# Performance work log

Hardware: AMD Instinct MI355X
Metric: run time of the kernel (lower is better)

The kernel has to match this reference:

```python
import jax, jax.numpy as jnp
import numpy as np

IN_DIM = 256
OUT_DIM = 64
NUM_HEADS = 4
N = 6144


def setup_inputs() -> dict:
    key = jax.random.key(0)
    ks = jax.random.split(key, 9)
    h = jax.random.normal(ks[0], (N, IN_DIM), dtype=jnp.float32)
    # dense multiplicative adjacency weights, one [N,N] matrix per head
    adj = jax.random.uniform(ks[1], (NUM_HEADS, N, N), dtype=jnp.float32)
    s = 1.0 / np.sqrt(IN_DIM)
    WQ = jax.random.normal(ks[2], (NUM_HEADS, IN_DIM, OUT_DIM), dtype=jnp.float32) * s
    WK = jax.random.normal(ks[3], (NUM_HEADS, IN_DIM, OUT_DIM), dtype=jnp.float32) * s
    WV = jax.random.normal(ks[4], (NUM_HEADS, IN_DIM, OUT_DIM), dtype=jnp.float32) * s
    bQ = jax.random.normal(ks[5], (NUM_HEADS, OUT_DIM), dtype=jnp.float32) * 0.01
    bK = jax.random.normal(ks[6], (NUM_HEADS, OUT_DIM), dtype=jnp.float32) * 0.01
    bV = jax.random.normal(ks[7], (NUM_HEADS, OUT_DIM), dtype=jnp.float32) * 0.01
    return {"adj": adj, "h": h, "WQ": WQ, "bQ": bQ, "WK": WK, "bK": bK, "WV": WV, "bV": bV}


def reference(adj, h, WQ, bQ, WK, bK, WV, bV):
    # Per-head projections, batched over heads: [H, N, out_dim]
    Qh = jnp.einsum('nd,hdo->hno', h, WQ) + bQ[:, None, :]
    Kh = jnp.einsum('nd,hdo->hno', h, WK) + bK[:, None, :]
    Vh = jnp.einsum('nd,hdo->hno', h, WV) + bV[:, None, :]
    scale = 1.0 / jnp.sqrt(jnp.asarray(h.shape[1], dtype=h.dtype))
    # multiplicative adjacency mask (NOT additive) applied before softmax
    A_tilde = scale * jnp.einsum('hno,hmo->hnm', Qh, Kh) * adj  # [H, N, N]
    attention = jax.nn.softmax(A_tilde, axis=-1)
    X = jnp.einsum('hnm,hmo->hno', attention, Vh)  # [H, N, out_dim]
    return X
```

## Files before the change

kernel.cpp:

```cpp
#include <hip/hip_runtime.h>
#include <hip/hip_bf16.h>

#define NN 6144
#define HEADS 4
#define DIN 256
#define DOUT 64

typedef __bf16 bf16_t;
typedef bf16_t bf16x8 __attribute__((ext_vector_type(8)));
typedef float f32x16 __attribute__((ext_vector_type(16)));
typedef float f32x4 __attribute__((ext_vector_type(4)));
typedef unsigned u32x4 __attribute__((ext_vector_type(4)));

#if __has_builtin(__builtin_amdgcn_exp2f)
#define EXP2(x) __builtin_amdgcn_exp2f(x)
#else
#define EXP2(x) exp2f(x)
#endif

static __device__ __forceinline__ f32x16 zero16() {
  f32x16 z;
#pragma unroll
  for (int i = 0; i < 16; ++i) z[i] = 0.0f;
  return z;
}

static __device__ __forceinline__ bf16x8 ldg8(const bf16_t* p) {
  return *reinterpret_cast<const bf16x8*>(p);
}

static __device__ __forceinline__ unsigned pk2(float a, float b) {
  union { bf16_t h[2]; unsigned u; } z;
  z.h[0] = (bf16_t)a;
  z.h[1] = (bf16_t)b;
  return z.u;
}

static __device__ __forceinline__ void pswap(unsigned& x, unsigned& y) {
  asm("v_permlane32_swap_b32 %0, %1" : "+v"(x), "+v"(y));
}

static __device__ __forceinline__ void gload_lds16(const float* g, float* lds) {
  __builtin_amdgcn_global_load_lds(
      (const __attribute__((address_space(1))) unsigned*)(uintptr_t)g,
      (__attribute__((address_space(3))) unsigned*)(unsigned)(uintptr_t)lds,
      16, 0, 0);
}

__global__ __launch_bounds__(256) void prep_kernel(
    const float* __restrict__ h, const float* __restrict__ WQ,
    const float* __restrict__ WK, const float* __restrict__ WV,
    bf16_t* __restrict__ hb, bf16_t* __restrict__ Wt) {
  int stride = gridDim.x * blockDim.x;
  int idx = blockIdx.x * blockDim.x + threadIdx.x;
  for (int i = idx; i < NN * DIN; i += stride)
    hb[i] = (bf16_t)h[i];
  const float c2 = 0.0625f * 1.4426950408889634f;
  for (int i = idx; i < 3 * HEADS * DOUT * DIN; i += stride) {
    int d = i & (DIN - 1);
    int o = (i >> 8) & (DOUT - 1);
    int hh = (i >> 14) & (HEADS - 1);
    int m = i >> 16;
    const float* W = (m == 0) ? WQ : (m == 1) ? WK : WV;
    float v = W[(hh * DIN + d) * DOUT + o];
    if (m == 0) v *= c2;
    Wt[i] = (bf16_t)v;
  }
}

__global__ __launch_bounds__(256) void proj_kernel(
    const bf16_t* __restrict__ hb, const bf16_t* __restrict__ Wt,
    const float* __restrict__ bQ, const float* __restrict__ bK,
    const float* __restrict__ bV,
    bf16_t* __restrict__ Qb, bf16_t* __restrict__ Kf, bf16_t* __restrict__ Vf) {
  const float c2 = 0.0625f * 1.4426950408889634f;
  int tid = threadIdx.x;
  int w = tid >> 6, l = tid & 63;
  int l31 = l & 31, lh = l >> 5;
  int hh = blockIdx.y;
  int n0 = blockIdx.x * 64;

#pragma unroll
  for (int s = 0; s < 3; ++s) {
    int t = w * 3 + s;
    if (t < 8) {
      int m = t >> 2;
      int rh = (t >> 1) & 1;
      int oh = t & 1;
      const bf16_t* arow = hb + (n0 + rh * 32 + l31) * DIN + 8 * lh;
      const bf16_t* brow = Wt + ((m * HEADS + hh) * DOUT + oh * 32 + l31) * DIN + 8 * lh;
      f32x16 acc = zero16();
#pragma unroll
      for (int kc = 0; kc < 16; ++kc)
        acc = __builtin_amdgcn_mfma_f32_32x32x16_bf16(ldg8(arow + kc * 16),
                                                      ldg8(brow + kc * 16), acc, 0, 0, 0);
      const float* bias = (m == 0) ? bQ : bK;
      float bv = bias[hh * DOUT + oh * 32 + l31];
      if (m == 0) {
        bv *= c2;
        bf16_t* outp = Qb + (size_t)(hh * NN + n0 + rh * 32) * DOUT + oh * 32 + l31;
#pragma unroll
        for (int r = 0; r < 16; ++r) {
          int q = (r & 3) + 8 * (r >> 2) + 4 * lh;
          outp[q * DOUT] = (bf16_t)(acc[r] + bv);
        }
      } else {
        int o = oh * 32 + l31;
        bf16_t* outp = Kf + (size_t)hh * 393216 + (n0 >> 6) * 4096 + rh * 2048 +
                       (o >> 4) * 512 + ((o >> 3) & 1) * 256 + (o & 7);
#pragma unroll
        for (int r = 0; r < 16; ++r) {
          int rr = (r & 3) + 8 * (r >> 2) + 4 * lh;
          outp[rr * 8] = (bf16_t)(acc[r] + bv);
        }
      }
    } else {
      int tt = t - 8;
      int oh = tt >> 1, nh = tt & 1;
      const bf16_t* arow = Wt + ((2 * HEADS + hh) * DOUT + oh * 32 + l31) * DIN + 8 * lh;
      const bf16_t* brow = hb + (n0 + nh * 32 + l31) * DIN + 8 * lh;
      f32x16 acc = zero16();
#pragma unroll
      for (int kc = 0; kc < 16; ++kc)
        acc = __builtin_amdgcn_mfma_f32_32x32x16_bf16(ldg8(arow + kc * 16),
                                                      ldg8(brow + kc * 16), acc, 0, 0, 0);
      int keyloc = nh * 32 + l31;
      bf16_t* outp = Vf + (size_t)hh * 393216 + (n0 >> 6) * 4096 + oh * 2048 +
                     (keyloc >> 4) * 512 + ((keyloc >> 3) & 1) * 256 + (keyloc & 7);
#pragma unroll
      for (int r = 0; r < 16; ++r) {
        int rr = (r & 3) + 8 * (r >> 2) + 4 * lh;
        float bvv = bV[hh * DOUT + oh * 32 + rr];
        outp[rr * 8] = (bf16_t)(acc[r] + bvv);
      }
    }
  }
}

__global__ __launch_bounds__(256, 2) void attn_kernel(
    const float* __restrict__ adj, const bf16_t* __restrict__ Qb,
    const bf16_t* __restrict__ Kf, const bf16_t* __restrict__ Vf,
    float* __restrict__ out) {
  __shared__ __align__(16) float smem[2][32][256];

  int tid = threadIdx.x;
  int w = tid >> 6, l = tid & 63;
  int l31 = l & 31, lh = l >> 5;
  int hh = blockIdx.y;
  int q0 = blockIdx.x * 32;

  const bf16_t* Qrow = Qb + (size_t)(hh * NN + q0 + l31) * DOUT + 8 * lh;
  bf16x8 qf[4];
#pragma unroll
  for (int kc = 0; kc < 4; ++kc) qf[kc] = ldg8(Qrow + kc * 16);

  const bf16_t* Kh = Kf + (size_t)hh * 393216;
  const bf16_t* Vh = Vf + (size_t)hh * 393216;
  const float* adjq = adj + (size_t)hh * NN * NN + (size_t)q0 * NN;

  f32x16 o0 = zero16(), o1 = zero16();
  float sacc = 0.0f;

#pragma unroll
  for (int i = 0; i < 8; ++i) {
    int row = 8 * w + i;
    gload_lds16(adjq + (size_t)row * NN + ((l ^ i) << 2), &smem[0][row][0]);
  }

  for (int it = 0; it < 24; ++it) {
    int cur = it & 1;
    int chunk = it * 4 + w;

    const bf16_t* kbase = Kh + (size_t)chunk * 4096 + l * 8;
    const bf16_t* vbase = Vh + (size_t)chunk * 4096 + l * 8;
    bf16x8 kf[8], vf[8];
#pragma unroll
    for (int x = 0; x < 4; ++x) {
      kf[x] = ldg8(kbase + x * 512);
      kf[4 + x] = ldg8(kbase + 2048 + x * 512);
    }
#pragma unroll
    for (int x = 0; x < 4; ++x) {
      vf[x] = ldg8(vbase + x * 512);
      vf[4 + x] = ldg8(vbase + 2048 + x * 512);
    }
    __builtin_amdgcn_sched_barrier(0);

    asm volatile("s_waitcnt vmcnt(16)" ::: "memory");
    __builtin_amdgcn_sched_barrier(0);
    __builtin_amdgcn_s_barrier();
    __builtin_amdgcn_sched_barrier(0);

    int nt = (it + 1 < 24) ? it + 1 : 23;
#pragma unroll
    for (int i = 0; i < 8; ++i) {
      int row = 8 * w + i;
      gload_lds16(adjq + (size_t)row * NN + nt * 256 + ((l ^ i) << 2),
                  &smem[cur ^ 1][row][0]);
    }
    __builtin_amdgcn_sched_barrier(0);

    f32x4 av[8];
#pragma unroll
    for (int t2 = 0; t2 < 2; ++t2)
#pragma unroll
      for (int g = 0; g < 4; ++g) {
        int c = 16 * w + 8 * t2 + 2 * g + lh;
        av[t2 * 4 + g] =
            *reinterpret_cast<const f32x4*>(&smem[cur][l31][(c ^ (l31 & 7)) << 2]);
      }

    f32x16 s0 = zero16(), s1 = zero16();
#pragma unroll
    for (int kc = 0; kc < 4; ++kc) {
      s0 = __builtin_amdgcn_mfma_f32_32x32x16_bf16(kf[kc], qf[kc], s0, 0, 0, 0);
      s1 = __builtin_amdgcn_mfma_f32_32x32x16_bf16(kf[4 + kc], qf[kc], s1, 0, 0, 0);
    }

#pragma unroll
    for (int t2 = 0; t2 < 2; ++t2) {
      f32x16 st = t2 ? s1 : s0;
      float p[16];
#pragma unroll
      for (int r = 0; r < 16; ++r) {
        float pv = EXP2(st[r] * av[4 * t2 + (r >> 2)][r & 3]);
        p[r] = pv;
        sacc += pv;
      }
#pragma unroll
      for (int c = 0; c < 2; ++c) {
        unsigned wA0 = pk2(p[8 * c + 0], p[8 * c + 1]);
        unsigned wB0 = pk2(p[8 * c + 2], p[8 * c + 3]);
        unsigned wA1 = pk2(p[8 * c + 4], p[8 * c + 5]);
        unsigned wB1 = pk2(p[8 * c + 6], p[8 * c + 7]);
        pswap(wA0, wA1);
        pswap(wB0, wB1);
        u32x4 pw;
        pw[0] = wA0; pw[1] = wB0; pw[2] = wA1; pw[3] = wB1;
        bf16x8 pb = __builtin_bit_cast(bf16x8, pw);
        int kc = 2 * t2 + c;
        o0 = __builtin_amdgcn_mfma_f32_32x32x16_bf16(vf[kc], pb, o0, 0, 0, 0);
        o1 = __builtin_amdgcn_mfma_f32_32x32x16_bf16(vf[4 + kc], pb, o1, 0, 0, 0);
      }
    }
  }

  asm volatile("s_waitcnt vmcnt(0)" ::: "memory");
  __syncthreads();

  float stot = sacc + __shfl_xor(sacc, 32);
  float* opart = &smem[0][0][0];
  float* ssum = &smem[0][0][0] + 8192;
  if (l < 32) ssum[w * 32 + l31] = stot;
#pragma unroll
  for (int r = 0; r < 16; ++r) {
    int d = (r & 3) + 8 * (r >> 2) + 4 * lh;
    opart[w * 2048 + d * 32 + l31] = o0[r];
    opart[w * 2048 + (32 + d) * 32 + l31] = o1[r];
  }
  __syncthreads();

#pragma unroll
  for (int k = 0; k < 8; ++k) {
    int idx = k * 256 + tid;
    int q = idx & 31, d = idx >> 5;
    float s = ssum[q] + ssum[32 + q] + ssum[64 + q] + ssum[96 + q];
    float ov = opart[d * 32 + q] + opart[2048 + d * 32 + q] +
               opart[4096 + d * 32 + q] + opart[6144 + d * 32 + q];
    out[(size_t)(hh * NN + q0 + q) * DOUT + d] = ov / s;
  }
}

extern "C" void kernel_launch(void* const* d_in, const int* in_sizes, int n_in,
                              void* d_out, int out_size, void* d_ws, size_t ws_size,
                              hipStream_t stream) {
  const float* adj = (const float*)d_in[0];
  const float* h   = (const float*)d_in[1];
  const float* WQ  = (const float*)d_in[2];
  const float* bQ  = (const float*)d_in[3];
  const float* WK  = (const float*)d_in[4];
  const float* bK  = (const float*)d_in[5];
  const float* WV  = (const float*)d_in[6];
  const float* bV  = (const float*)d_in[7];
  float* out = (float*)d_out;

  if (ws_size < 12976128) return;

  char* ws = (char*)d_ws;
  bf16_t* hb = (bf16_t*)ws;
  bf16_t* Wt = (bf16_t*)(ws + 3145728);
  bf16_t* Qb = (bf16_t*)(ws + 3538944);
  bf16_t* Kf = (bf16_t*)(ws + 6684672);
  bf16_t* Vf = (bf16_t*)(ws + 9830400);

  prep_kernel<<<1024, 256, 0, stream>>>(h, WQ, WK, WV, hb, Wt);
  proj_kernel<<<dim3(96, 4), 256, 0, stream>>>(hb, Wt, bQ, bK, bV, Qb, Kf, Vf);
  attn_kernel<<<dim3(192, 4), 256, 0, stream>>>(adj, Qb, Kf, Vf, out);
}
```

Measured before the change: 188.0 us.

## Split attention key range across single-wave blocks with atomic accumulation and normalize pass

```diff
diff --git a/kernel.cpp b/kernel.cpp
--- a/kernel.cpp
+++ b/kernel.cpp
@@ -50,11 +50,13 @@
 __global__ __launch_bounds__(256) void prep_kernel(
     const float* __restrict__ h, const float* __restrict__ WQ,
     const float* __restrict__ WK, const float* __restrict__ WV,
-    bf16_t* __restrict__ hb, bf16_t* __restrict__ Wt) {
+    bf16_t* __restrict__ hb, bf16_t* __restrict__ Wt,
+    float* __restrict__ out, float* __restrict__ denom) {
   int stride = gridDim.x * blockDim.x;
   int idx = blockIdx.x * blockDim.x + threadIdx.x;
-  for (int i = idx; i < NN * DIN; i += stride)
-    hb[i] = (bf16_t)h[i];
+  for (int i = idx; i < HEADS * NN * DOUT; i += stride) out[i] = 0.0f;
+  for (int i = idx; i < HEADS * NN; i += stride) denom[i] = 0.0f;
+  for (int i = idx; i < NN * DIN; i += stride) hb[i] = (bf16_t)h[i];
   const float c2 = 0.0625f * 1.4426950408889634f;
   for (int i = idx; i < 3 * HEADS * DOUT * DIN; i += stride) {
     int d = i & (DIN - 1);
@@ -124,9 +126,9 @@
       for (int kc = 0; kc < 16; ++kc)
         acc = __builtin_amdgcn_mfma_f32_32x32x16_bf16(ldg8(arow + kc * 16),
                                                       ldg8(brow + kc * 16), acc, 0, 0, 0);
-      int keyloc = nh * 32 + l31;
+      int k6 = nh * 32 + l31;
       bf16_t* outp = Vf + (size_t)hh * 393216 + (n0 >> 6) * 4096 + oh * 2048 +
-                     (keyloc >> 4) * 512 + ((keyloc >> 3) & 1) * 256 + (keyloc & 7);
+                     (k6 >> 4) * 512 + ((k6 >> 3) & 1) * 256 + (k6 & 7);
 #pragma unroll
       for (int r = 0; r < 16; ++r) {
         int rr = (r & 3) + 8 * (r >> 2) + 4 * lh;
@@ -137,17 +139,23 @@
   }
 }
 
-__global__ __launch_bounds__(256, 2) void attn_kernel(
+__global__ __launch_bounds__(64, 2) void attn_kernel(
     const float* __restrict__ adj, const bf16_t* __restrict__ Qb,
     const bf16_t* __restrict__ Kf, const bf16_t* __restrict__ Vf,
-    float* __restrict__ out) {
-  __shared__ __align__(16) float smem[2][32][256];
-
-  int tid = threadIdx.x;
-  int w = tid >> 6, l = tid & 63;
+    float* __restrict__ out, float* __restrict__ denom) {
+  __shared__ __align__(16) float tile[2][32][64];
+
+  int l = threadIdx.x;
   int l31 = l & 31, lh = l >> 5;
-  int hh = blockIdx.y;
-  int q0 = blockIdx.x * 32;
+
+  int bid = blockIdx.x;
+  int sb = (bid & 7) * 384 + (bid >> 3);
+  int bx = sb % 192;
+  int rem = sb / 192;
+  int ky = rem & 3;
+  int hh = rem >> 2;
+  int q0 = bx * 32;
+  int ck0 = ky * 24;
 
   const bf16_t* Qrow = Qb + (size_t)(hh * NN + q0 + l31) * DOUT + 8 * lh;
   bf16x8 qf[4];
@@ -156,20 +164,24 @@
 
   const bf16_t* Kh = Kf + (size_t)hh * 393216;
   const bf16_t* Vh = Vf + (size_t)hh * 393216;
-  const float* adjq = adj + (size_t)hh * NN * NN + (size_t)q0 * NN;
+  const float* adjbase = adj + (size_t)(hh * NN + q0) * NN + ky * 1536;
+
+#define STAGE(BUF, CK)                                                      \
+  _Pragma("unroll") for (int i = 0; i < 8; ++i) {                           \
+    int row = 4 * i + (l >> 4);                                             \
+    int sc = (l & 15) ^ (row & 15);                                         \
+    gload_lds16(adjbase + (size_t)row * NN + (CK) * 64 + sc * 4,            \
+                &tile[BUF][4 * i][0]);                                      \
+  }
 
   f32x16 o0 = zero16(), o1 = zero16();
   float sacc = 0.0f;
 
-#pragma unroll
-  for (int i = 0; i < 8; ++i) {
-    int row = 8 * w + i;
-    gload_lds16(adjq + (size_t)row * NN + ((l ^ i) << 2), &smem[0][row][0]);
-  }
+  STAGE(0, 0)
 
   for (int it = 0; it < 24; ++it) {
-    int cur = it & 1;
-    int chunk = it * 4 + w;
+    int buf = it & 1;
+    int chunk = ck0 + it;
 
     const bf16_t* kbase = Kh + (size_t)chunk * 4096 + l * 8;
     const bf16_t* vbase = Vh + (size_t)chunk * 4096 + l * 8;
@@ -186,28 +198,21 @@
     }
     __builtin_amdgcn_sched_barrier(0);
 
-    asm volatile("s_waitcnt vmcnt(16)" ::: "memory");
+    int nt = (it + 1 < 24) ? it + 1 : 23;
+    STAGE(buf ^ 1, nt)
     __builtin_amdgcn_sched_barrier(0);
-    __builtin_amdgcn_s_barrier();
+
+    asm volatile("s_waitcnt vmcnt(24)" ::: "memory");
     __builtin_amdgcn_sched_barrier(0);
 
-    int nt = (it + 1 < 24) ? it + 1 : 23;
-#pragma unroll
-    for (int i = 0; i < 8; ++i) {
-      int row = 8 * w + i;
-      gload_lds16(adjq + (size_t)row * NN + nt * 256 + ((l ^ i) << 2),
-                  &smem[cur ^ 1][row][0]);
-    }
-    __builtin_amdgcn_sched_barrier(0);
-
     f32x4 av[8];
 #pragma unroll
     for (int t2 = 0; t2 < 2; ++t2)
 #pragma unroll
       for (int g = 0; g < 4; ++g) {
-        int c = 16 * w + 8 * t2 + 2 * g + lh;
+        int c = 8 * t2 + 2 * g + lh;
         av[t2 * 4 + g] =
-            *reinterpret_cast<const f32x4*>(&smem[cur][l31][(c ^ (l31 & 7)) << 2]);
+            *reinterpret_cast<const f32x4*>(&tile[buf][l31][(c ^ (l31 & 15)) << 2]);
       }
 
     f32x16 s0 = zero16(), s1 = zero16();
@@ -239,36 +244,33 @@
         pw[0] = wA0; pw[1] = wB0; pw[2] = wA1; pw[3] = wB1;
         bf16x8 pb = __builtin_bit_cast(bf16x8, pw);
         int kc = 2 * t2 + c;
-        o0 = __builtin_amdgcn_mfma_f32_32x32x16_bf16(vf[kc], pb, o0, 0, 0, 0);
-        o1 = __builtin_amdgcn_mfma_f32_32x32x16_bf16(vf[4 + kc], pb, o1, 0, 0, 0);
-      }
-    }
-  }
-
-  asm volatile("s_waitcnt vmcnt(0)" ::: "memory");
-  __syncthreads();
+        o0 = __builtin_amdgcn_mfma_f32_32x32x16_bf16(pb, vf[kc], o0, 0, 0, 0);
+        o1 = __builtin_amdgcn_mfma_f32_32x32x16_bf16(pb, vf[4 + kc], o1, 0, 0, 0);
+      }
+    }
+  }
 
   float stot = sacc + __shfl_xor(sacc, 32);
-  float* opart = &smem[0][0][0];
-  float* ssum = &smem[0][0][0] + 8192;
-  if (l < 32) ssum[w * 32 + l31] = stot;
+  if (l < 32) atomicAdd(&denom[hh * NN + q0 + l31], stot);
 #pragma unroll
   for (int r = 0; r < 16; ++r) {
-    int d = (r & 3) + 8 * (r >> 2) + 4 * lh;
-    opart[w * 2048 + d * 32 + l31] = o0[r];
-    opart[w * 2048 + (32 + d) * 32 + l31] = o1[r];
-  }
-  __syncthreads();
-
-#pragma unroll
-  for (int k = 0; k < 8; ++k) {
-    int idx = k * 256 + tid;
-    int q = idx & 31, d = idx >> 5;
-    float s = ssum[q] + ssum[32 + q] + ssum[64 + q] + ssum[96 + q];
-    float ov = opart[d * 32 + q] + opart[2048 + d * 32 + q] +
-               opart[4096 + d * 32 + q] + opart[6144 + d * 32 + q];
-    out[(size_t)(hh * NN + q0 + q) * DOUT + d] = ov / s;
-  }
+    int q = (r & 3) + 8 * (r >> 2) + 4 * lh;
+    size_t base = (size_t)(hh * NN + q0 + q) * DOUT;
+    atomicAdd(&out[base + l31], o0[r]);
+    atomicAdd(&out[base + 32 + l31], o1[r]);
+  }
+#undef STAGE
+}
+
+__global__ __launch_bounds__(256) void norm_kernel(
+    float* __restrict__ out, const float* __restrict__ denom) {
+  int i = blockIdx.x * 256 + threadIdx.x;
+  float dn = denom[i >> 4];
+  f32x4 v = reinterpret_cast<f32x4*>(out)[i];
+  float inv = 1.0f / dn;
+#pragma unroll
+  for (int j = 0; j < 4; ++j) v[j] *= inv;
+  reinterpret_cast<f32x4*>(out)[i] = v;
 }
 
 extern "C" void kernel_launch(void* const* d_in, const int* in_sizes, int n_in,
@@ -284,16 +286,18 @@
   const float* bV  = (const float*)d_in[7];
   float* out = (float*)d_out;
 
-  if (ws_size < 12976128) return;
+  if (ws_size < 13074432) return;
 
   char* ws = (char*)d_ws;
-  bf16_t* hb = (bf16_t*)ws;
-  bf16_t* Wt = (bf16_t*)(ws + 3145728);
-  bf16_t* Qb = (bf16_t*)(ws + 3538944);
-  bf16_t* Kf = (bf16_t*)(ws + 6684672);
-  bf16_t* Vf = (bf16_t*)(ws + 9830400);
-
-  prep_kernel<<<1024, 256, 0, stream>>>(h, WQ, WK, WV, hb, Wt);
+  bf16_t* hb    = (bf16_t*)ws;
+  bf16_t* Wt    = (bf16_t*)(ws + 3145728);
+  bf16_t* Qb    = (bf16_t*)(ws + 3538944);
+  bf16_t* Kf    = (bf16_t*)(ws + 6684672);
+  bf16_t* Vf    = (bf16_t*)(ws + 9830400);
+  float*  denom = (float*)(ws + 12976128);
+
+  prep_kernel<<<1024, 256, 0, stream>>>(h, WQ, WK, WV, hb, Wt, out, denom);
   proj_kernel<<<dim3(96, 4), 256, 0, stream>>>(hb, Wt, bQ, bK, bV, Qb, Kf, Vf);
-  attn_kernel<<<dim3(192, 4), 256, 0, stream>>>(adj, Qb, Kf, Vf, out);
-}
+  attn_kernel<<<3072, 64, 0, stream>>>(adj, Qb, Kf, Vf, out, denom);
+  norm_kernel<<<1536, 256, 0, stream>>>(out, denom);
+}
```

After: 201.1 us. +6.9%, slower.
